# Optimization experiments

Hardware: AMD Instinct MI355X
Metric: run time of the kernel (lower is better)

Reference implementation:

```python
import jax, jax.numpy as jnp
import numpy as np

B, S, D, H, HD = 2, 2048, 1024, 16, 64


def setup_inputs() -> dict:
    key = jax.random.key(0)
    ks = jax.random.split(key, 5)
    sc = 1.0 / np.sqrt(D)  # lecun-normal-ish scale for kernels
    return {
        "x": jax.random.normal(ks[0], (B, S, D), jnp.float32),
        "Wq": jax.random.normal(ks[1], (D, H, HD), jnp.float32) * sc,
        "bq": jnp.zeros((H, HD), jnp.float32),
        "Wk": jax.random.normal(ks[2], (D, H, HD), jnp.float32) * sc,
        "bk": jnp.zeros((H, HD), jnp.float32),
        "Wv": jax.random.normal(ks[3], (D, H, HD), jnp.float32) * sc,
        "bv": jnp.zeros((H, HD), jnp.float32),
        "Wo": jax.random.normal(ks[4], (H, HD, D), jnp.float32) * (1.0 / np.sqrt(H * HD)),
        "bo": jnp.zeros((D,), jnp.float32),
    }


def reference(x, Wq, bq, Wk, bk, Wv, bv, Wo, bo):
    # QKV projections: [B,S,D] x [D,H,Hd] -> [B,S,H,Hd]
    q = jnp.einsum("bsd,dhk->bshk", x, Wq) + bq
    k = jnp.einsum("bsd,dhk->bshk", x, Wk) + bk
    v = jnp.einsum("bsd,dhk->bshk", x, Wv) + bv
    depth = q.shape[-1]
    q = q / jnp.sqrt(jnp.asarray(depth, q.dtype))
    # attention weights [B,H,Sq,Sk]
    attn = jnp.einsum("bqhd,bkhd->bhqk", q, k)
    attn = jax.nn.softmax(attn, axis=-1)
    # weighted values [B,Sq,H,Hd]
    out = jnp.einsum("bhqk,bkhd->bqhd", attn, v)
    # output projection back to d_model
    return jnp.einsum("bqhd,hdm->bqm", out, Wo) + bo
```

## Files before the change

### kernel.cpp

```cpp
#include <hip/hip_runtime.h>


typedef __attribute__((ext_vector_type(8))) short short8;
typedef __attribute__((ext_vector_type(4))) float float4v;
typedef __attribute__((ext_vector_type(16))) float f32x16;
typedef __attribute__((ext_vector_type(2))) int int2v;

__device__ __forceinline__ void async16(void* lds, const void* g) {
  __builtin_amdgcn_global_load_lds(
      (__attribute__((address_space(1))) void*)(g),
      (__attribute__((address_space(3))) void*)(lds), 16, 0, 0);
}

__device__ __forceinline__ short f2bf(float f) {
  union { float f; unsigned u; } v;
  v.f = f;
  unsigned r = v.u + 0x7fffu + ((v.u >> 16) & 1u);
  return (short)(r >> 16);
}

#if __has_builtin(__builtin_amdgcn_cvt_pk_bf16_f32)
__device__ __forceinline__ unsigned pk2(float a, float b) {
  auto h = __builtin_amdgcn_cvt_pk_bf16_f32(a, b);
  unsigned u;
  __builtin_memcpy(&u, &h, 4);
  return u;
}
#else
__device__ __forceinline__ unsigned pk2(float a, float b) {
  return (unsigned)(unsigned short)f2bf(a) |
         ((unsigned)(unsigned short)f2bf(b) << 16);
}
#endif

#if __has_builtin(__builtin_amdgcn_exp2f)
__device__ __forceinline__ float fexp2(float x) { return __builtin_amdgcn_exp2f(x); }
#else
__device__ __forceinline__ float fexp2(float x) { return exp2f(x); }
#endif

__device__ __forceinline__ void plswap(unsigned& a, unsigned& b) {
#if __has_builtin(__builtin_amdgcn_permlane32_swap)
  int2v r = __builtin_amdgcn_permlane32_swap((int)a, (int)b, false, false);
  a = (unsigned)r[0];
  b = (unsigned)r[1];
#else
  unsigned ax = (unsigned)__shfl_xor((int)a, 32);
  unsigned bx = (unsigned)__shfl_xor((int)b, 32);
  bool hh = (threadIdx.x & 32) != 0;
  a = hh ? bx : a;
  b = hh ? b : ax;
#endif
}

__device__ __forceinline__ short8 mk8(unsigned a, unsigned b, unsigned c,
                                      unsigned d) {
  union { unsigned u[4]; short8 s; } r;
  r.u[0] = a; r.u[1] = b; r.u[2] = c; r.u[3] = d;
  return r.s;
}

__device__ __forceinline__ short8 cvt8(const float* __restrict__ g) {
  float4v a = *(const float4v*)(g);
  float4v b = *(const float4v*)(g + 4);
  union { unsigned u[4]; short8 s; } r;
  r.u[0] = pk2(a[0], a[1]);
  r.u[1] = pk2(a[2], a[3]);
  r.u[2] = pk2(b[0], b[1]);
  r.u[3] = pk2(b[2], b[3]);
  return r.s;
}

__device__ __forceinline__ void mfma_tile(const short* As, const short* Bs,
                                          float4v acc[4][4]) {
  int t = threadIdx.x, lane = t & 63, w = t >> 6, r = lane & 15, q = lane >> 4;
  int wr = (w >> 1) * 64, wc = (w & 1) * 64;
  short8 af[4], bfr[4];
#pragma unroll
  for (int mt = 0; mt < 4; mt++)
    af[mt] = *(const short8*)(As + (wr + mt * 16 + r) * 32 + q * 8);
#pragma unroll
  for (int nt = 0; nt < 4; nt++)
    bfr[nt] = *(const short8*)(Bs + (wc + nt * 16 + r) * 32 + q * 8);
#pragma unroll
  for (int mt = 0; mt < 4; mt++)
#pragma unroll
    for (int nt = 0; nt < 4; nt++)
      acc[mt][nt] = __builtin_amdgcn_mfma_f32_16x16x32_bf16(
          af[mt], bfr[nt], acc[mt][nt], 0, 0, 0);
}

__global__ __launch_bounds__(256) void conv_wx(
    const float* __restrict__ W0, const float* __restrict__ W1,
    const float* __restrict__ W2, const float* __restrict__ x,
    short* __restrict__ WT, short* __restrict__ xb) {
  __shared__ short tile[64][65];
  int b = blockIdx.x;
  int t = threadIdx.x;
  if (b < 2048) {
    int i = (b * 256 + t) * 8;
    *(short8*)(xb + i) = cvt8(x + i);
    return;
  }
  int wb = b - 2048;
  int z = wb >> 8;
  int rem = wb & 255;
  const float* src = (z == 0) ? W0 : (z == 1) ? W1 : W2;
  short* d = WT + z * 1048576;
  int r0 = (rem >> 4) * 64, c0 = (rem & 15) * 64;
#pragma unroll
  for (int i = 0; i < 16; i++) {
    int e = i * 256 + t;
    int r = e >> 6, c = e & 63;
    tile[r][c] = f2bf(src[(r0 + r) * 1024 + c0 + c]);
  }
  __syncthreads();
#pragma unroll
  for (int i = 0; i < 16; i++) {
    int e = i * 256 + t;
    int r = e >> 6, c = e & 63;
    d[(c0 + r) * 1024 + r0 + c] = tile[c][r];
  }
}

__global__ __launch_bounds__(256) void convwo_t(
    const float* __restrict__ W, short* __restrict__ d) {
  __shared__ short tile[64][65];
  int r0 = blockIdx.y * 64, c0 = blockIdx.x * 64;
  int t = threadIdx.x;
#pragma unroll
  for (int i = 0; i < 16; i++) {
    int e = i * 256 + t;
    int r = e >> 6, c = e & 63;
    tile[r][c] = f2bf(W[(r0 + r) * 1024 + c0 + c]);
  }
  __syncthreads();
#pragma unroll
  for (int i = 0; i < 16; i++) {
    int e = i * 256 + t;
    int r = e >> 6, c = e & 63;
    d[(c0 + r) * 1024 + r0 + c] = tile[c][r];
  }
}

__global__ __launch_bounds__(256, 2) void qkv_gemm_fast(
    const short* __restrict__ xb, const short* __restrict__ WT,
    const float* __restrict__ bq, const float* __restrict__ bk,
    const float* __restrict__ bv, short* __restrict__ Qd,
    short* __restrict__ Kd, short* __restrict__ Vt0, short* __restrict__ Vt1) {
  __shared__ __align__(16) short As[4096];
  __shared__ __align__(16) short Bs[4096];
  int z = blockIdx.z;
  int t = threadIdx.x;
  int m0, n0;
  if (z < 2) { m0 = blockIdx.y * 128; n0 = blockIdx.x * 128; }
  else       { m0 = blockIdx.x * 128; n0 = blockIdx.y * 128; }
  const short* Wz = WT + z * 1048576;
  const short* A = (z < 2) ? xb : Wz;
  const short* B = (z < 2) ? Wz : xb;
  float4v acc[4][4];
#pragma unroll
  for (int mt = 0; mt < 4; mt++)
#pragma unroll
    for (int nt = 0; nt < 4; nt++)
#pragma unroll
      for (int k = 0; k < 4; k++) acc[mt][nt][k] = 0.0f;

  for (int kt = 0; kt < 32; kt++) {
    int k0 = kt * 32;
    __syncthreads();
#pragma unroll
    for (int i = 0; i < 2; i++) {
      int p = i * 256 + t;
      int rr = p >> 2, cc = p & 3;
      async16(As + p * 8, A + (m0 + rr) * 1024 + k0 + cc * 8);
      async16(Bs + p * 8, B + (n0 + rr) * 1024 + k0 + cc * 8);
    }
    __syncthreads();
    mfma_tile(As, Bs, acc);
  }
  int lane = t & 63, w = t >> 6, r = lane & 15, q = lane >> 4;
  int wr = (w >> 1) * 64, wc = (w & 1) * 64;
  if (z < 2) {
    const float* bias = (z == 0) ? bq : bk;
    short* dst = (z == 0) ? Qd : Kd;
    float scale = (z == 0) ? 0.1803368801111204f : 1.0f;
#pragma unroll
    for (int mt = 0; mt < 4; mt++)
#pragma unroll
      for (int reg = 0; reg < 4; reg++) {
        int m = m0 + wr + mt * 16 + q * 4 + reg;
        int b = m >> 11, s = m & 2047;
#pragma unroll
        for (int nt = 0; nt < 4; nt++) {
          int n = n0 + wc + nt * 16 + r;
          int h = n >> 6, hd = n & 63;
          float v = (acc[mt][nt][reg] + bias[n]) * scale;
          dst[((b * 16 + h) << 17) + (s << 6) + hd] = f2bf(v);
        }
      }
  } else {
#pragma unroll
    for (int mt = 0; mt < 4; mt++)
#pragma unroll
      for (int reg = 0; reg < 4; reg++) {
        int mrow = m0 + wr + mt * 16 + q * 4 + reg;
        int h = mrow >> 6, hd = mrow & 63;
        float bias = bv[mrow];
#pragma unroll
        for (int nt = 0; nt < 4; nt++) {
          int n = n0 + wc + nt * 16 + r;
          int b = n >> 11, s = n & 2047;
          int idx = b * 16 + h;
          short* vp = (idx < 16) ? (Vt0 + idx * 131072)
                                 : (Vt1 + (idx - 16) * 131072);
          vp[(hd << 11) + s] = f2bf(acc[mt][nt][reg] + bias);
        }
      }
  }
}

__device__ __forceinline__ void stage_kv(short* Ksb, short* Vsb,
                                         const short* Kt, const short* Vt,
                                         int t) {
#pragma unroll
  for (int i = 0; i < 2; i++) {
    int p = i * 256 + t, rr = p >> 3, c = p & 7, cs = (c ^ (rr & 7)) * 8;
    async16(Ksb + p * 8, Kt + rr * 64 + cs);
    async16(Vsb + p * 8, Vt + rr * 2048 + cs);
  }
}

#define ATTN_BODY(FIRST, LAST, KT, SIN, SOUT)                                 \
  {                                                                           \
    if (!(LAST))                                                              \
      stage_kv(SM + (((KT) + 1) & 1) * 4096,                                  \
               SM + 8192 + (((KT) + 1) & 1) * 4096, Kb + ((KT) + 1) * 4096,   \
               Vb + ((KT) + 1) * 64, t);                                      \
    short8 pa[2];                                                             \
    if (!(FIRST)) {                                                           \
      float pvv[16];                                                          \
      _Pragma("unroll") for (int i = 0; i < 16; i++) pvv[i] = fexp2(SIN[i]);  \
      lsum += (((pvv[0] + pvv[1]) + (pvv[2] + pvv[3])) +                      \
               ((pvv[4] + pvv[5]) + (pvv[6] + pvv[7]))) +                     \
              (((pvv[8] + pvv[9]) + (pvv[10] + pvv[11])) +                    \
               ((pvv[12] + pvv[13]) + (pvv[14] + pvv[15])));                  \
      unsigned u0 = pk2(pvv[0], pvv[1]), u1 = pk2(pvv[2], pvv[3]);            \
      unsigned u2 = pk2(pvv[4], pvv[5]), u3 = pk2(pvv[6], pvv[7]);            \
      unsigned u4 = pk2(pvv[8], pvv[9]), u5 = pk2(pvv[10], pvv[11]);          \
      unsigned u6 = pk2(pvv[12], pvv[13]), u7 = pk2(pvv[14], pvv[15]);        \
      plswap(u0, u2);                                                         \
      plswap(u1, u3);                                                         \
      plswap(u4, u6);                                                         \
      plswap(u5, u7);                                                         \
      pa[0] = mk8(u0, u1, u2, u3);                                            \
      pa[1] = mk8(u4, u5, u6, u7);                                            \
    }                                                                         \
    const short* Kc = SM + ((KT) & 1) * 4096;                                 \
    const short* Vc = SM + 8192 + ((KT) & 1) * 4096;                          \
    int kr = kh * 32 + l31;                                                   \
    short8 ka[4];                                                             \
    _Pragma("unroll") for (int ds = 0; ds < 4; ds++) ka[ds] =                 \
        *(const short8*)(Kc + kr * 64 + (((ds * 2 + hi) ^ (kr & 7)) * 8));    \
    _Pragma("unroll") for (int i = 0; i < 16; i++) SOUT[i] = 0.0f;            \
    __builtin_amdgcn_s_setprio(1);                                            \
    _Pragma("unroll") for (int ds = 0; ds < 4; ds++) SOUT =                   \
        __builtin_amdgcn_mfma_f32_32x32x16_bf16(ka[ds], qf[ds], SOUT, 0, 0,   \
                                                0);                           \
    if (!(FIRST)) {                                                           \
      _Pragma("unroll") for (int ks = 0; ks < 2; ks++)                        \
          _Pragma("unroll") for (int ht = 0; ht < 2; ht++) oacc[ht] =         \
          __builtin_amdgcn_mfma_f32_32x32x16_bf16(pa[ks], vbr[ks * 2 + ht],   \
                                                  oacc[ht], 0, 0, 0);         \
    }                                                                         \
    __builtin_amdgcn_s_setprio(0);                                            \
    _Pragma("unroll") for (int ks = 0; ks < 2; ks++)                          \
        _Pragma("unroll") for (int ht = 0; ht < 2; ht++) {                    \
      int d = ht * 32 + l31;                                                  \
      vbr[ks * 2 + ht] = *(const short8*)(                                    \
          Vc + d * 64 + (((kh * 4 + ks * 2 + hi) ^ (d & 7)) * 8));            \
    }                                                                         \
    __syncthreads();                                                          \
  }

__global__ __launch_bounds__(256, 4) void attn_kernel(
    short* __restrict__ QO, const short* __restrict__ K,
    const short* __restrict__ V0, const short* __restrict__ V1) {
  __shared__ __align__(16) short SM[16640];
  float* sums = (float*)(SM + 16384);
  float* xl = (float*)(SM + 16512);
  float* xo = (float*)SM;
  int id = blockIdx.x;
  int chunk = id >> 3;
  int bh = (id & 7) * 4 + (chunk >> 5);
  int qt = chunk & 31;
  int t = threadIdx.x, lane = t & 63, w = t >> 6;
  int l31 = lane & 31, hi = lane >> 5;
  int qsel = w & 1, kh = w >> 1;
  short* Qb = QO + bh * 131072;
  const short* Kb = K + bh * 131072;
  const short* Vb = (bh < 16) ? (V0 + bh * 131072) : (V1 + (bh - 16) * 131072);
  int q0w = qt * 64 + qsel * 32;

  short8 qf[4];
#pragma unroll
  for (int ds = 0; ds < 4; ds++)
    qf[ds] = *(const short8*)(Qb + (q0w + l31) * 64 + ds * 16 + hi * 8);

  f32x16 oacc[2];
  f32x16 sA, sB;
  short8 vbr[4];
#pragma unroll
  for (int ht = 0; ht < 2; ht++)
#pragma unroll
    for (int i = 0; i < 16; i++) oacc[ht][i] = 0.0f;
  float lsum = 0.0f;

  stage_kv(SM, SM + 8192, Kb, Vb, t);
  __syncthreads();

  ATTN_BODY(true, false, 0, sB, sA);
  for (int kt = 1; kt < 31; kt += 2) {
    ATTN_BODY(false, false, kt, sA, sB);
    ATTN_BODY(false, false, kt + 1, sB, sA);
  }
  ATTN_BODY(false, true, 31, sA, sB);

  {
    float pvv[16];
#pragma unroll
    for (int i = 0; i < 16; i++) pvv[i] = fexp2(sB[i]);
    lsum += (((pvv[0] + pvv[1]) + (pvv[2] + pvv[3])) +
             ((pvv[4] + pvv[5]) + (pvv[6] + pvv[7]))) +
            (((pvv[8] + pvv[9]) + (pvv[10] + pvv[11])) +
             ((pvv[12] + pvv[13]) + (pvv[14] + pvv[15])));
    unsigned u0 = pk2(pvv[0], pvv[1]), u1 = pk2(pvv[2], pvv[3]);
    unsigned u2 = pk2(pvv[4], pvv[5]), u3 = pk2(pvv[6], pvv[7]);
    unsigned u4 = pk2(pvv[8], pvv[9]), u5 = pk2(pvv[10], pvv[11]);
    unsigned u6 = pk2(pvv[12], pvv[13]), u7 = pk2(pvv[14], pvv[15]);
    plswap(u0, u2);
    plswap(u1, u3);
    plswap(u4, u6);
    plswap(u5, u7);
    short8 pa0 = mk8(u0, u1, u2, u3);
    short8 pa1 = mk8(u4, u5, u6, u7);
#pragma unroll
    for (int ht = 0; ht < 2; ht++)
      oacc[ht] = __builtin_amdgcn_mfma_f32_32x32x16_bf16(pa0, vbr[ht],
                                                         oacc[ht], 0, 0, 0);
#pragma unroll
    for (int ht = 0; ht < 2; ht++)
      oacc[ht] = __builtin_amdgcn_mfma_f32_32x32x16_bf16(pa1, vbr[2 + ht],
                                                         oacc[ht], 0, 0, 0);
  }

  float lt = lsum + __shfl_xor(lsum, 32);
  float* xb = xo + (qsel * 64 + lane) * 33;
  if (kh == 1) {
#pragma unroll
    for (int i = 0; i < 16; i++) xb[i] = oacc[0][i];
#pragma unroll
    for (int i = 0; i < 16; i++) xb[16 + i] = oacc[1][i];
    if (lane < 32) xl[qsel * 32 + l31] = lt;
  }
  __syncthreads();
  if (kh == 0) {
#pragma unroll
    for (int i = 0; i < 16; i++) oacc[0][i] += xb[i];
#pragma unroll
    for (int i = 0; i < 16; i++) oacc[1][i] += xb[16 + i];
    float ltot = lt + xl[qsel * 32 + l31];
    float inv = 1.0f / fmaxf(ltot, 1.0e-30f);
    if (lane < 32) sums[qsel * 32 + l31] = inv;
    __builtin_amdgcn_s_waitcnt(0xC07F);
#pragma unroll
    for (int rg = 0; rg < 16; rg++) {
      int srow = (rg & 3) + 8 * (rg >> 2) + 4 * hi;
      float invr = sums[qsel * 32 + srow];
      short* orow = Qb + (q0w + srow) * 64;
      orow[l31] = f2bf(oacc[0][rg] * invr);
      orow[32 + l31] = f2bf(oacc[1][rg] * invr);
    }
  }
}

__global__ __launch_bounds__(256, 2) void out_gemm(
    const short* __restrict__ O, const short* __restrict__ WoT,
    const float* __restrict__ bo, float* __restrict__ out) {
  __shared__ __align__(16) short As[4096];
  __shared__ __align__(16) short Bs[2048];
  int m0 = blockIdx.y * 128, n0 = blockIdx.x * 64;
  int t = threadIdx.x, lane = t & 63, w = t >> 6, r = lane & 15, q = lane >> 4;
  int wr = (w >> 1) * 64, wc = (w & 1) * 32;
  float4v acc[4][2];
#pragma unroll
  for (int mt = 0; mt < 4; mt++)
#pragma unroll
    for (int nt = 0; nt < 2; nt++)
#pragma unroll
      for (int k = 0; k < 4; k++) acc[mt][nt][k] = 0.0f;

  for (int kt = 0; kt < 32; kt++) {
    int k0 = kt * 32;
    int h0 = k0 >> 6, hd0 = k0 & 63;
    __syncthreads();
#pragma unroll
    for (int i = 0; i < 2; i++) {
      int p = i * 256 + t;
      int rr = p >> 2, cc = p & 3;
      int m = m0 + rr;
      async16(As + p * 8, O + (m >> 11) * 2097152 + h0 * 131072 +
                              (m & 2047) * 64 + hd0 + cc * 8);
    }
    {
      int rr = t >> 2, cc = t & 3;
      async16(Bs + t * 8, WoT + (n0 + rr) * 1024 + k0 + cc * 8);
    }
    __syncthreads();
    short8 af[4], bfr[2];
#pragma unroll
    for (int mt = 0; mt < 4; mt++)
      af[mt] = *(const short8*)(As + (wr + mt * 16 + r) * 32 + q * 8);
#pragma unroll
    for (int nt = 0; nt < 2; nt++)
      bfr[nt] = *(const short8*)(Bs + (wc + nt * 16 + r) * 32 + q * 8);
#pragma unroll
    for (int mt = 0; mt < 4; mt++)
#pragma unroll
      for (int nt = 0; nt < 2; nt++)
        acc[mt][nt] = __builtin_amdgcn_mfma_f32_16x16x32_bf16(
            af[mt], bfr[nt], acc[mt][nt], 0, 0, 0);
  }
#pragma unroll
  for (int mt = 0; mt < 4; mt++)
#pragma unroll
    for (int reg = 0; reg < 4; reg++) {
      int m = m0 + wr + mt * 16 + q * 4 + reg;
#pragma unroll
      for (int nt = 0; nt < 2; nt++) {
        int n = n0 + wc + nt * 16 + r;
        out[m * 1024 + n] = acc[mt][nt][reg] + bo[n];
      }
    }
}

extern "C" void kernel_launch(void* const* d_in, const int* in_sizes, int n_in,
                              void* d_out, int out_size, void* d_ws,
                              size_t ws_size, hipStream_t stream) {
  (void)in_sizes; (void)n_in; (void)out_size; (void)ws_size;
  const float* x = (const float*)d_in[0];
  const float* Wq = (const float*)d_in[1];
  const float* bq = (const float*)d_in[2];
  const float* Wk = (const float*)d_in[3];
  const float* bk = (const float*)d_in[4];
  const float* Wv = (const float*)d_in[5];
  const float* bv = (const float*)d_in[6];
  const float* Wo = (const float*)d_in[7];
  const float* bo = (const float*)d_in[8];
  float* out = (float*)d_out;
  char* ws = (char*)d_ws;
  short* QO  = (short*)(ws);
  short* Kws = (short*)(ws + (8u << 20));
  short* WoT = (short*)(ws + (8u << 20));
  short* xb  = (short*)d_out;
  short* WT  = (short*)d_out + 4 * 1048576;
  short* Vt0 = (short*)Wq;
  short* Vt1 = (short*)Wk;

  dim3 tb(256);
  conv_wx<<<dim3(2816), tb, 0, stream>>>(Wq, Wk, Wv, x, WT, xb);
  qkv_gemm_fast<<<dim3(8, 32, 3), tb, 0, stream>>>(xb, WT, bq, bk, bv,
                                                   QO, Kws, Vt0, Vt1);
  attn_kernel<<<dim3(1024), tb, 0, stream>>>(QO, Kws, Vt0, Vt1);
  convwo_t<<<dim3(16, 16), tb, 0, stream>>>(Wo, WoT);
  out_gemm<<<dim3(16, 32), tb, 0, stream>>>(QO, WoT, bo, out);
}
```

Measured before the change: 225.4 us.

## Load K/V fragments directly from global into registers, dropping LDS staging

Replaces the async global-to-LDS double-buffered K/V staging and per-tile barriers with direct global loads of MFMA fragments into registers, software-pipelined one tile ahead. Each wave loads its own K rows and V columns, which removes the __syncthreads per key tile and the LDS round trip. The trade-off is that waves sharing the same K/V now each fetch it from global/L2 instead of sharing one LDS copy. The loads are also less coalesced, and load latency is exposed with only one tile of prefetch.

```diff
diff --git a/kernel.cpp b/kernel.cpp
--- a/kernel.cpp
+++ b/kernel.cpp
@@ -220,76 +220,54 @@
   }
 }
 
-__device__ __forceinline__ void stage_kv(short* Ksb, short* Vsb,
-                                         const short* Kt, const short* Vt,
-                                         int t) {
-#pragma unroll
-  for (int i = 0; i < 2; i++) {
-    int p = i * 256 + t, rr = p >> 3, c = p & 7, cs = (c ^ (rr & 7)) * 8;
-    async16(Ksb + p * 8, Kt + rr * 64 + cs);
-    async16(Vsb + p * 8, Vt + rr * 2048 + cs);
-  }
-}
-
-#define ATTN_BODY(FIRST, LAST, KT, SIN, SOUT)                                 \
-  {                                                                           \
-    if (!(LAST))                                                              \
-      stage_kv(SM + (((KT) + 1) & 1) * 4096,                                  \
-               SM + 8192 + (((KT) + 1) & 1) * 4096, Kb + ((KT) + 1) * 4096,   \
-               Vb + ((KT) + 1) * 64, t);                                      \
-    short8 pa[2];                                                             \
-    if (!(FIRST)) {                                                           \
-      float pvv[16];                                                          \
-      _Pragma("unroll") for (int i = 0; i < 16; i++) pvv[i] = fexp2(SIN[i]);  \
-      lsum += (((pvv[0] + pvv[1]) + (pvv[2] + pvv[3])) +                      \
-               ((pvv[4] + pvv[5]) + (pvv[6] + pvv[7]))) +                     \
-              (((pvv[8] + pvv[9]) + (pvv[10] + pvv[11])) +                    \
-               ((pvv[12] + pvv[13]) + (pvv[14] + pvv[15])));                  \
-      unsigned u0 = pk2(pvv[0], pvv[1]), u1 = pk2(pvv[2], pvv[3]);            \
-      unsigned u2 = pk2(pvv[4], pvv[5]), u3 = pk2(pvv[6], pvv[7]);            \
-      unsigned u4 = pk2(pvv[8], pvv[9]), u5 = pk2(pvv[10], pvv[11]);          \
-      unsigned u6 = pk2(pvv[12], pvv[13]), u7 = pk2(pvv[14], pvv[15]);        \
-      plswap(u0, u2);                                                         \
-      plswap(u1, u3);                                                         \
-      plswap(u4, u6);                                                         \
-      plswap(u5, u7);                                                         \
-      pa[0] = mk8(u0, u1, u2, u3);                                            \
-      pa[1] = mk8(u4, u5, u6, u7);                                            \
-    }                                                                         \
-    const short* Kc = SM + ((KT) & 1) * 4096;                                 \
-    const short* Vc = SM + 8192 + ((KT) & 1) * 4096;                          \
-    int kr = kh * 32 + l31;                                                   \
-    short8 ka[4];                                                             \
-    _Pragma("unroll") for (int ds = 0; ds < 4; ds++) ka[ds] =                 \
-        *(const short8*)(Kc + kr * 64 + (((ds * 2 + hi) ^ (kr & 7)) * 8));    \
-    _Pragma("unroll") for (int i = 0; i < 16; i++) SOUT[i] = 0.0f;            \
-    __builtin_amdgcn_s_setprio(1);                                            \
-    _Pragma("unroll") for (int ds = 0; ds < 4; ds++) SOUT =                   \
-        __builtin_amdgcn_mfma_f32_32x32x16_bf16(ka[ds], qf[ds], SOUT, 0, 0,   \
-                                                0);                           \
-    if (!(FIRST)) {                                                           \
-      _Pragma("unroll") for (int ks = 0; ks < 2; ks++)                        \
-          _Pragma("unroll") for (int ht = 0; ht < 2; ht++) oacc[ht] =         \
-          __builtin_amdgcn_mfma_f32_32x32x16_bf16(pa[ks], vbr[ks * 2 + ht],   \
-                                                  oacc[ht], 0, 0, 0);         \
-    }                                                                         \
-    __builtin_amdgcn_s_setprio(0);                                            \
-    _Pragma("unroll") for (int ks = 0; ks < 2; ks++)                          \
-        _Pragma("unroll") for (int ht = 0; ht < 2; ht++) {                    \
-      int d = ht * 32 + l31;                                                  \
-      vbr[ks * 2 + ht] = *(const short8*)(                                    \
-          Vc + d * 64 + (((kh * 4 + ks * 2 + hi) ^ (d & 7)) * 8));            \
-    }                                                                         \
-    __syncthreads();                                                          \
-  }
+__device__ __forceinline__ void attn_compute(const short8 ka[4],
+                                             const short8 vb[4],
+                                             const short8 qf[4],
+                                             f32x16 oacc[2], float& lsum) {
+  f32x16 sacc;
+#pragma unroll
+  for (int i = 0; i < 16; i++) sacc[i] = 0.0f;
+  __builtin_amdgcn_s_setprio(1);
+#pragma unroll
+  for (int ds = 0; ds < 4; ds++)
+    sacc = __builtin_amdgcn_mfma_f32_32x32x16_bf16(ka[ds], qf[ds], sacc,
+                                                   0, 0, 0);
+  __builtin_amdgcn_s_setprio(0);
+  float pvv[16];
+#pragma unroll
+  for (int i = 0; i < 16; i++) pvv[i] = fexp2(sacc[i]);
+  lsum += (((pvv[0] + pvv[1]) + (pvv[2] + pvv[3])) +
+           ((pvv[4] + pvv[5]) + (pvv[6] + pvv[7]))) +
+          (((pvv[8] + pvv[9]) + (pvv[10] + pvv[11])) +
+           ((pvv[12] + pvv[13]) + (pvv[14] + pvv[15])));
+  unsigned u0 = pk2(pvv[0], pvv[1]), u1 = pk2(pvv[2], pvv[3]);
+  unsigned u2 = pk2(pvv[4], pvv[5]), u3 = pk2(pvv[6], pvv[7]);
+  unsigned u4 = pk2(pvv[8], pvv[9]), u5 = pk2(pvv[10], pvv[11]);
+  unsigned u6 = pk2(pvv[12], pvv[13]), u7 = pk2(pvv[14], pvv[15]);
+  plswap(u0, u2);
+  plswap(u1, u3);
+  plswap(u4, u6);
+  plswap(u5, u7);
+  short8 pa0 = mk8(u0, u1, u2, u3);
+  short8 pa1 = mk8(u4, u5, u6, u7);
+  __builtin_amdgcn_s_setprio(1);
+#pragma unroll
+  for (int ht = 0; ht < 2; ht++)
+    oacc[ht] = __builtin_amdgcn_mfma_f32_32x32x16_bf16(pa0, vb[ht],
+                                                       oacc[ht], 0, 0, 0);
+#pragma unroll
+  for (int ht = 0; ht < 2; ht++)
+    oacc[ht] = __builtin_amdgcn_mfma_f32_32x32x16_bf16(pa1, vb[2 + ht],
+                                                       oacc[ht], 0, 0, 0);
+  __builtin_amdgcn_s_setprio(0);
+}
 
 __global__ __launch_bounds__(256, 4) void attn_kernel(
     short* __restrict__ QO, const short* __restrict__ K,
     const short* __restrict__ V0, const short* __restrict__ V1) {
-  __shared__ __align__(16) short SM[16640];
-  float* sums = (float*)(SM + 16384);
-  float* xl = (float*)(SM + 16512);
-  float* xo = (float*)SM;
+  __shared__ __align__(16) float xo[2 * 64 * 33];
+  __shared__ float xl[64];
+  __shared__ float sums[64];
   int id = blockIdx.x;
   int chunk = id >> 3;
   int bh = (id & 7) * 4 + (chunk >> 5);
@@ -307,52 +285,41 @@
   for (int ds = 0; ds < 4; ds++)
     qf[ds] = *(const short8*)(Qb + (q0w + l31) * 64 + ds * 16 + hi * 8);
 
+  const short* kp = Kb + (kh * 32 + l31) * 64 + hi * 8;
+  const short* vp = Vb + l31 * 2048 + kh * 32 + hi * 8;
+
+#define LOADK(dst, KT)                                                  \
+  {                                                                     \
+    _Pragma("unroll") for (int ds = 0; ds < 4; ds++) dst[ds] =          \
+        *(const short8*)(kp + (KT) * 4096 + ds * 16);                   \
+  }
+#define LOADV(dst, KT)                                                  \
+  {                                                                     \
+    _Pragma("unroll") for (int ks = 0; ks < 2; ks++)                    \
+        _Pragma("unroll") for (int ht = 0; ht < 2; ht++)                \
+            dst[ks * 2 + ht] = *(const short8*)(vp + (KT) * 64 +        \
+                                                ks * 16 + ht * 65536);  \
+  }
+
   f32x16 oacc[2];
-  f32x16 sA, sB;
-  short8 vbr[4];
 #pragma unroll
   for (int ht = 0; ht < 2; ht++)
 #pragma unroll
     for (int i = 0; i < 16; i++) oacc[ht][i] = 0.0f;
   float lsum = 0.0f;
 
-  stage_kv(SM, SM + 8192, Kb, Vb, t);
-  __syncthreads();
-
-  ATTN_BODY(true, false, 0, sB, sA);
-  for (int kt = 1; kt < 31; kt += 2) {
-    ATTN_BODY(false, false, kt, sA, sB);
-    ATTN_BODY(false, false, kt + 1, sB, sA);
-  }
-  ATTN_BODY(false, true, 31, sA, sB);
-
-  {
-    float pvv[16];
-#pragma unroll
-    for (int i = 0; i < 16; i++) pvv[i] = fexp2(sB[i]);
-    lsum += (((pvv[0] + pvv[1]) + (pvv[2] + pvv[3])) +
-             ((pvv[4] + pvv[5]) + (pvv[6] + pvv[7]))) +
-            (((pvv[8] + pvv[9]) + (pvv[10] + pvv[11])) +
-             ((pvv[12] + pvv[13]) + (pvv[14] + pvv[15])));
-    unsigned u0 = pk2(pvv[0], pvv[1]), u1 = pk2(pvv[2], pvv[3]);
-    unsigned u2 = pk2(pvv[4], pvv[5]), u3 = pk2(pvv[6], pvv[7]);
-    unsigned u4 = pk2(pvv[8], pvv[9]), u5 = pk2(pvv[10], pvv[11]);
-    unsigned u6 = pk2(pvv[12], pvv[13]), u7 = pk2(pvv[14], pvv[15]);
-    plswap(u0, u2);
-    plswap(u1, u3);
-    plswap(u4, u6);
-    plswap(u5, u7);
-    short8 pa0 = mk8(u0, u1, u2, u3);
-    short8 pa1 = mk8(u4, u5, u6, u7);
-#pragma unroll
-    for (int ht = 0; ht < 2; ht++)
-      oacc[ht] = __builtin_amdgcn_mfma_f32_32x32x16_bf16(pa0, vbr[ht],
-                                                         oacc[ht], 0, 0, 0);
-#pragma unroll
-    for (int ht = 0; ht < 2; ht++)
-      oacc[ht] = __builtin_amdgcn_mfma_f32_32x32x16_bf16(pa1, vbr[2 + ht],
-                                                         oacc[ht], 0, 0, 0);
-  }
+  short8 kaA[4], kaB[4], vbA[4], vbB[4];
+  LOADK(kaA, 0);
+  for (int kt = 0; kt < 32; kt += 2) {
+    LOADV(vbA, kt);
+    LOADK(kaB, kt + 1);
+    attn_compute(kaA, vbA, qf, oacc, lsum);
+    LOADV(vbB, kt + 1);
+    if (kt + 2 < 32) LOADK(kaA, kt + 2);
+    attn_compute(kaB, vbB, qf, oacc, lsum);
+  }
+#undef LOADK
+#undef LOADV
 
   float lt = lsum + __shfl_xor(lsum, 32);
   float* xb = xo + (qsel * 64 + lane) * 33;
```

After: 299.7 us. 33.0% more time.
